# Optimization experiments

Measured on AMD Instinct MI355X. Metric: run time of the kernel, lower is better.

Reference implementation:

```python
import jax, jax.numpy as jnp
import numpy as np

L, B, E, H = 512, 32, 1024, 16
NEG = -1e9  # finite stand-in for masked_fill(-inf); avoids NaNs if a row were fully masked


def setup_inputs() -> dict:
    key = jax.random.key(0)
    ks = jax.random.split(key, 6)
    s_in = (2.0 / (3 * E + E)) ** 0.5   # xavier-ish scale for in_proj
    s_out = (2.0 / (E + E)) ** 0.5
    return {
        "query": jax.random.normal(ks[0], (L, B, E), jnp.float32),
        "key": jax.random.normal(ks[1], (L, B, E), jnp.float32),
        "value": jax.random.normal(ks[2], (L, B, E), jnp.float32),
        "attn_mask": jax.random.randint(ks[3], (B, L, L), 0, 2).astype(jnp.bool_),
        "in_proj_weight": jax.random.normal(ks[4], (3 * E, E), jnp.float32) * s_in,
        "in_proj_bias": jnp.zeros((3 * E,), jnp.float32),
        "out_proj_weight": jax.random.normal(ks[5], (E, E), jnp.float32) * s_out,
        "out_proj_bias": jnp.zeros((E,), jnp.float32),
        "num_heads": H,
    }


def reference(query, key, value, attn_mask, in_proj_weight, in_proj_bias,
              out_proj_weight, out_proj_bias, num_heads):
    Lq, Bz, Em = query.shape
    hd = Em // num_heads
    Wq, Wk, Wv = jnp.split(in_proj_weight, 3, axis=0)
    bq, bk, bv = jnp.split(in_proj_bias, 3, axis=0)
    # in-projection: x @ W^T + b  (torch F.linear convention)
    q = query @ Wq.T + bq
    k = key @ Wk.T + bk
    v = value @ Wv.T + bv
    # [L, B, E] -> [B*H, L, hd], batch-major (b*H + h) per torch view semantics
    def split_heads(x):
        return x.reshape(x.shape[0], Bz * num_heads, hd).transpose(1, 0, 2)
    q, k, v = split_heads(q), split_heads(k), split_heads(v)
    q = q / jnp.sqrt(jnp.asarray(hd, q.dtype))
    # scores: [B*H, Lq, Lk]
    attn = jnp.einsum('bqd,bkd->bqk', q, k)
    # mask broadcast to heads: [B, L, L] -> [B*H, L, L] with index b*H + h
    mask_mh = jnp.repeat(attn_mask, num_heads, axis=0)
    # original: scatter zeros where masked, then masked_fill(-inf) inside
    # multi_head_positional_attention; net effect = mask -> -inf before softmax
    attn = jnp.where(mask_mh, NEG, attn)
    p = jax.nn.softmax(attn, axis=-1)
    out = jnp.einsum('bqk,bkd->bqd', p, v)        # [B*H, Lq, hd]
    out = out.transpose(1, 0, 2).reshape(Lq, Bz, Em)
    out = out @ out_proj_weight.T + out_proj_bias  # [L, B, E]
    return out
```

## Files before the change

kernel.cpp:

```cpp
#include <hip/hip_runtime.h>
#include <hip/hip_bf16.h>
#include <stdint.h>

#define LSEQ 512
#define BATCH 32
#define EMB 1024
#define NHEAD 16
#define HDIM 64
#define TOK (LSEQ*BATCH)
#define BHTOT (BATCH*NHEAD)

typedef __attribute__((ext_vector_type(8))) short short8;
typedef __attribute__((ext_vector_type(4))) short short4v;
typedef __attribute__((ext_vector_type(4))) float f32x4;

__device__ __forceinline__ short f2bf(float f) {
  __hip_bfloat16 h = __float2bfloat16(f);
  union { __hip_bfloat16 h; short s; } u; u.h = h;
  return u.s;
}

#if defined(__has_builtin)
#if __has_builtin(__builtin_amdgcn_global_load_lds)
#define HAVE_GLL 1
#endif
#endif

__device__ __forceinline__ void gload_lds16(const void* g, void* l) {
#ifdef HAVE_GLL
  __builtin_amdgcn_global_load_lds((const __attribute__((address_space(1))) void*)g,
                                   (__attribute__((address_space(3))) void*)l, 16, 0, 0);
#else
  *(short8*)l = *(const short8*)g;
#endif
}

__global__ void cast_weights(const float* __restrict__ W, const float* __restrict__ Wo,
                             const float* __restrict__ bias,
                             short* __restrict__ Wb, short* __restrict__ Wob,
                             float* __restrict__ biasp)
{
  int i = blockIdx.x * 256 + threadIdx.x;
  if (i < 786432) {
    f32x4 v = ((const f32x4*)W)[i];
    int row = i >> 8;
    float s = (row < 1024) ? 0.125f : 1.0f;
    short4v o;
    o[0] = f2bf(v[0]*s); o[1] = f2bf(v[1]*s); o[2] = f2bf(v[2]*s); o[3] = f2bf(v[3]*s);
    ((short4v*)Wb)[i] = o;
  } else {
    int j = i - 786432;
    f32x4 v = ((const f32x4*)Wo)[j];
    short4v o;
    o[0] = f2bf(v[0]); o[1] = f2bf(v[1]); o[2] = f2bf(v[2]); o[3] = f2bf(v[3]);
    ((short4v*)Wob)[j] = o;
  }
  if (i < 768) {
    f32x4 v = ((const f32x4*)bias)[i];
    float s = (i < 256) ? 0.125f : 1.0f;
    f32x4 o = {v[0]*s, v[1]*s, v[2]*s, v[3]*s};
    ((f32x4*)biasp)[i] = o;
  }
}

__global__ void maskbits_kernel(const int* __restrict__ mask, uint32_t* __restrict__ mb)
{
  int w = (blockIdx.x * 256 + threadIdx.x) >> 6;
  int lane = threadIdx.x & 63;
  const int* src = mask + ((size_t)w << 9);
  uint32_t* dst = mb + w * 16;
  #pragma unroll
  for (int c = 0; c < 8; ++c) {
    int v = src[c * 64 + lane];
    unsigned long long m = __ballot(v != 0);
    if (lane == 0) dst[c*2]     = (uint32_t)m;
    if (lane == 1) dst[c*2 + 1] = (uint32_t)(m >> 32);
  }
}

__launch_bounds__(256, 4)
__global__ void proj_gemm(const float* __restrict__ Aq, const float* __restrict__ Ak,
                          const float* __restrict__ Av, const short* __restrict__ W,
                          const float* __restrict__ biasp,
                          short* __restrict__ qh, short* __restrict__ kh,
                          short* __restrict__ vh)
{
  int z = blockIdx.z;
  const float* A = (z == 0) ? Aq : (z == 1) ? Ak : Av;
  short* C       = (z == 0) ? qh : (z == 1) ? kh : vh;
  const short* B = W + (size_t)z * 1024 * 1024;
  const float* bp = biasp + z * 1024;

  int flat = blockIdx.y * 8 + blockIdx.x;
  int X = flat & 7, s = flat >> 3;
  int m0 = (X * 16 + (s >> 3)) * 128;
  int n0 = (s & 7) * 128;

  __shared__ alignas(16) short As[128 * 32];
  __shared__ alignas(16) short Bs[128 * 32];

  const int tid = threadIdx.x, lane = tid & 63;
  const int w = tid >> 6;
  const int wm = (w >> 1) * 64, wn = (w & 1) * 64;
  const int l15 = lane & 15, l4 = lane >> 4;

  f32x4 acc[4][4];
  #pragma unroll
  for (int mi = 0; mi < 4; ++mi)
    #pragma unroll
    for (int ni = 0; ni < 4; ++ni) acc[mi][ni] = f32x4{0.f, 0.f, 0.f, 0.f};

  for (int k0 = 0; k0 < 1024; k0 += 32) {
    __syncthreads();
    #pragma unroll
    for (int jj = 0; jj < 2; ++jj) {
      int ch = tid + jj * 256;
      int row = ch >> 2, cl = ch & 3;
      int sw = (row >> 1) & 3;
      int cs = cl ^ sw;
      const float* ga = A + (size_t)(m0 + row) * 1024 + k0 + cl * 8;
      f32x4 x0 = *(const f32x4*)ga;
      f32x4 x1 = *(const f32x4*)(ga + 4);
      short8 o;
      o[0] = f2bf(x0[0]); o[1] = f2bf(x0[1]); o[2] = f2bf(x0[2]); o[3] = f2bf(x0[3]);
      o[4] = f2bf(x1[0]); o[5] = f2bf(x1[1]); o[6] = f2bf(x1[2]); o[7] = f2bf(x1[3]);
      *(short8*)&As[row * 32 + cs * 8] = o;
      const short* gb = B + (size_t)(n0 + row) * 1024 + k0 + cs * 8;
      gload_lds16(gb, &Bs[ch * 8]);
    }
    __syncthreads();

    short8 af[4], bfr[4];
    #pragma unroll
    for (int mi = 0; mi < 4; ++mi) {
      int row = wm + mi * 16 + l15;
      int cs = l4 ^ ((row >> 1) & 3);
      af[mi] = *(const short8*)&As[row * 32 + cs * 8];
    }
    #pragma unroll
    for (int ni = 0; ni < 4; ++ni) {
      int row = wn + ni * 16 + l15;
      int cs = l4 ^ ((row >> 1) & 3);
      bfr[ni] = *(const short8*)&Bs[row * 32 + cs * 8];
    }
    #pragma unroll
    for (int mi = 0; mi < 4; ++mi)
      #pragma unroll
      for (int ni = 0; ni < 4; ++ni)
        acc[mi][ni] = __builtin_amdgcn_mfma_f32_16x16x32_bf16(af[mi], bfr[ni], acc[mi][ni], 0, 0, 0);
  }

  #pragma unroll
  for (int ni = 0; ni < 4; ++ni) {
    int gcol = n0 + wn + ni * 16 + l15;
    float bv = bp[gcol];
    int h = gcol >> 6, d = gcol & 63;
    #pragma unroll
    for (int mi = 0; mi < 4; ++mi) {
      int growb = m0 + wm + mi * 16 + l4 * 4;
      #pragma unroll
      for (int r = 0; r < 4; ++r) {
        int grow = growb + r;
        int lsq = grow >> 5, bb = grow & 31;
        C[((size_t)((bb * NHEAD + h) * LSEQ + lsq)) * HDIM + d] = f2bf(acc[mi][ni][r] + bv);
      }
    }
  }
}

__launch_bounds__(256, 2)
__global__ void attn_kernel(const short* __restrict__ qh, const short* __restrict__ kh,
                            const short* __restrict__ vh, const uint32_t* __restrict__ mb,
                            short* __restrict__ ao)
{
  int flat = blockIdx.y * 8 + blockIdx.x;
  int X = flat & 7, s = flat >> 3;
  int bh = X * 64 + (s >> 3);
  int qblk = s & 7;
  int b = bh >> 4, h = bh & 15;
  int q0 = qblk * 64;

  const int tid = threadIdx.x, lane = tid & 63, w = tid >> 6;
  const int l15 = lane & 15, l4 = lane >> 4;

  __shared__ alignas(16) short Ks[64 * 64];
  __shared__ alignas(16) short Vt[64 * 72];
  __shared__ alignas(16) short Ps[4 * 16 * 72];
  __shared__ uint32_t Mw[64 * 2];

  const size_t bhoff = (size_t)bh * (LSEQ * HDIM);

  short8 aq[2];
  {
    int qrow = q0 + w * 16 + l15;
    const short* qp = qh + bhoff + (size_t)qrow * HDIM + l4 * 8;
    aq[0] = *(const short8*)qp;
    aq[1] = *(const short8*)(qp + 32);
  }

  f32x4 oacc[4];
  #pragma unroll
  for (int n = 0; n < 4; ++n) oacc[n] = f32x4{0.f, 0.f, 0.f, 0.f};
  float m_i[4], l_i[4];
  #pragma unroll
  for (int r = 0; r < 4; ++r) { m_i[r] = -1e30f; l_i[r] = 0.f; }

  for (int kt = 0; kt < 8; ++kt) {
    __syncthreads();
    #pragma unroll
    for (int jj = 0; jj < 2; ++jj) {
      int ch = tid + jj * 256;
      int row = ch >> 3, cl = ch & 7;
      int cg = cl ^ (row & 7);
      const short* g = kh + bhoff + (size_t)(kt * 64 + row) * HDIM + cg * 8;
      gload_lds16(g, &Ks[ch * 8]);
    }
    #pragma unroll
    for (int jj = 0; jj < 2; ++jj) {
      int c = tid + jj * 256;
      int kv = c & 63, d0 = (c >> 6) * 8;
      const short* g = vh + bhoff + (size_t)(kt * 64 + kv) * HDIM + d0;
      short8 vv = *(const short8*)g;
      #pragma unroll
      for (int j = 0; j < 8; ++j) Vt[(d0 + j) * 72 + kv] = vv[j];
    }
    if (tid < 128) {
      int qr = tid >> 1, wd = tid & 1;
      Mw[qr * 2 + wd] = mb[((size_t)b * LSEQ + q0 + qr) * 16 + kt * 2 + wd];
    }
    __syncthreads();

    f32x4 sa[4];
    #pragma unroll
    for (int n = 0; n < 4; ++n) sa[n] = f32x4{0.f, 0.f, 0.f, 0.f};
    #pragma unroll
    for (int ss = 0; ss < 2; ++ss) {
      #pragma unroll
      for (int n = 0; n < 4; ++n) {
        int row = n * 16 + l15;
        int cs = (ss * 4 + l4) ^ (row & 7);
        short8 bk = *(const short8*)&Ks[row * 64 + cs * 8];
        sa[n] = __builtin_amdgcn_mfma_f32_16x16x32_bf16(aq[ss], bk, sa[n], 0, 0, 0);
      }
    }

    #pragma unroll
    for (int r = 0; r < 4; ++r) {
      int qr = w * 16 + l4 * 4 + r;
      uint32_t mlo = Mw[qr * 2], mhi = Mw[qr * 2 + 1];
      float sv[4];
      #pragma unroll
      for (int n = 0; n < 4; ++n) {
        int cc = n * 16 + l15;
        uint32_t bit = ((cc < 32 ? (mlo >> cc) : (mhi >> (cc - 32))) & 1u);
        sv[n] = bit ? -1e9f : sa[n][r];
      }
      float rmax = fmaxf(fmaxf(sv[0], sv[1]), fmaxf(sv[2], sv[3]));
      #pragma unroll
      for (int off = 1; off < 16; off <<= 1) rmax = fmaxf(rmax, __shfl_xor(rmax, off, 64));
      float mn = fmaxf(m_i[r], rmax);
      float sc = __expf(m_i[r] - mn);
      float p0 = __expf(sv[0] - mn), p1 = __expf(sv[1] - mn);
      float p2 = __expf(sv[2] - mn), p3 = __expf(sv[3] - mn);
      float rs = p0 + p1 + p2 + p3;
      #pragma unroll
      for (int off = 1; off < 16; off <<= 1) rs += __shfl_xor(rs, off, 64);
      l_i[r] = l_i[r] * sc + rs;
      m_i[r] = mn;
      #pragma unroll
      for (int n = 0; n < 4; ++n) oacc[n][r] *= sc;
      short* pp = &Ps[w * 1152 + (l4 * 4 + r) * 72];
      pp[0 * 16 + l15] = f2bf(p0);
      pp[1 * 16 + l15] = f2bf(p1);
      pp[2 * 16 + l15] = f2bf(p2);
      pp[3 * 16 + l15] = f2bf(p3);
    }

    #pragma unroll
    for (int ss = 0; ss < 2; ++ss) {
      short8 pa = *(const short8*)&Ps[w * 1152 + l15 * 72 + ss * 32 + l4 * 8];
      #pragma unroll
      for (int n = 0; n < 4; ++n) {
        short8 bv = *(const short8*)&Vt[(n * 16 + l15) * 72 + ss * 32 + l4 * 8];
        oacc[n] = __builtin_amdgcn_mfma_f32_16x16x32_bf16(pa, bv, oacc[n], 0, 0, 0);
      }
    }
  }

  #pragma unroll
  for (int r = 0; r < 4; ++r) {
    float inv = 1.0f / l_i[r];
    int qrow = q0 + w * 16 + l4 * 4 + r;
    size_t tbase = ((size_t)qrow * BATCH + b) * EMB + h * HDIM;
    #pragma unroll
    for (int n = 0; n < 4; ++n)
      ao[tbase + n * 16 + l15] = f2bf(oacc[n][r] * inv);
  }
}

__launch_bounds__(256, 4)
__global__ void out_gemm(const short* __restrict__ Ab, const short* __restrict__ W,
                         const float* __restrict__ bo, float* __restrict__ out)
{
  int flat = blockIdx.y * 8 + blockIdx.x;
  int X = flat & 7, s = flat >> 3;
  int m0 = (X * 16 + (s >> 3)) * 128;
  int n0 = (s & 7) * 128;

  __shared__ alignas(16) short As[128 * 32];
  __shared__ alignas(16) short Bs[128 * 32];

  const int tid = threadIdx.x, lane = tid & 63;
  const int w = tid >> 6;
  const int wm = (w >> 1) * 64, wn = (w & 1) * 64;
  const int l15 = lane & 15, l4 = lane >> 4;

  f32x4 acc[4][4];
  #pragma unroll
  for (int mi = 0; mi < 4; ++mi)
    #pragma unroll
    for (int ni = 0; ni < 4; ++ni) acc[mi][ni] = f32x4{0.f, 0.f, 0.f, 0.f};

  for (int k0 = 0; k0 < 1024; k0 += 32) {
    __syncthreads();
    #pragma unroll
    for (int jj = 0; jj < 2; ++jj) {
      int ch = tid + jj * 256;
      int row = ch >> 2, cl = ch & 3;
      int cs = cl ^ ((row >> 1) & 3);
      const short* ga = Ab + (size_t)(m0 + row) * 1024 + k0 + cs * 8;
      gload_lds16(ga, &As[ch * 8]);
      const short* gb = W + (size_t)(n0 + row) * 1024 + k0 + cs * 8;
      gload_lds16(gb, &Bs[ch * 8]);
    }
    __syncthreads();

    short8 af[4], bfr[4];
    #pragma unroll
    for (int mi = 0; mi < 4; ++mi) {
      int row = wm + mi * 16 + l15;
      int cs = l4 ^ ((row >> 1) & 3);
      af[mi] = *(const short8*)&As[row * 32 + cs * 8];
    }
    #pragma unroll
    for (int ni = 0; ni < 4; ++ni) {
      int row = wn + ni * 16 + l15;
      int cs = l4 ^ ((row >> 1) & 3);
      bfr[ni] = *(const short8*)&Bs[row * 32 + cs * 8];
    }
    #pragma unroll
    for (int mi = 0; mi < 4; ++mi)
      #pragma unroll
      for (int ni = 0; ni < 4; ++ni)
        acc[mi][ni] = __builtin_amdgcn_mfma_f32_16x16x32_bf16(af[mi], bfr[ni], acc[mi][ni], 0, 0, 0);
  }

  #pragma unroll
  for (int ni = 0; ni < 4; ++ni) {
    int gcol = n0 + wn + ni * 16 + l15;
    float bv = bo[gcol];
    #pragma unroll
    for (int mi = 0; mi < 4; ++mi) {
      int growb = m0 + wm + mi * 16 + l4 * 4;
      #pragma unroll
      for (int r = 0; r < 4; ++r)
        out[(size_t)(growb + r) * 1024 + gcol] = acc[mi][ni][r] + bv;
    }
  }
}

extern "C" void kernel_launch(void* const* d_in, const int* in_sizes, int n_in,
                              void* d_out, int out_size, void* d_ws, size_t ws_size,
                              hipStream_t stream) {
  const float* q_in = (const float*)d_in[0];
  const float* k_in = (const float*)d_in[1];
  const float* v_in = (const float*)d_in[2];
  const int*   mask = (const int*)d_in[3];
  const float* Wp   = (const float*)d_in[4];
  const float* bp   = (const float*)d_in[5];
  const float* Wo   = (const float*)d_in[6];
  const float* bo   = (const float*)d_in[7];

  char* ws = (char*)d_ws;
  short* Wb    = (short*)ws;    ws += (size_t)3072 * 1024 * 2;
  short* Wob   = (short*)ws;    ws += (size_t)1024 * 1024 * 2;
  float* biasp = (float*)ws;    ws += (size_t)3072 * 4;
  short* qh    = (short*)ws;    ws += (size_t)TOK * EMB * 2;
  short* kh    = (short*)ws;    ws += (size_t)TOK * EMB * 2;
  short* vh    = (short*)ws;    ws += (size_t)TOK * EMB * 2;
  short* ao    = (short*)ws;    ws += (size_t)TOK * EMB * 2;
  uint32_t* mb = (uint32_t*)ws; ws += (size_t)BATCH * LSEQ * 16 * 4;

  cast_weights<<<4096, 256, 0, stream>>>(Wp, Wo, bp, Wb, Wob, biasp);
  maskbits_kernel<<<4096, 256, 0, stream>>>(mask, mb);
  proj_gemm<<<dim3(8, 128, 3), 256, 0, stream>>>(q_in, k_in, v_in, Wb, biasp, qh, kh, vh);
  attn_kernel<<<dim3(8, 512), 256, 0, stream>>>(qh, kh, vh, mb, ao);
  out_gemm<<<dim3(8, 128), 256, 0, stream>>>(ao, Wob, bo, (float*)d_out);
}
```

Baseline: 357.7 us.

## Double-buffer LDS tiles in projection and output GEMMs to overlap loads with MFMA

Both projection and output GEMMs now use two LDS buffers per operand. The next K-slice is prefetched (global_load_lds for bf16 operands, register loads plus a deferred bf16 conversion for fp32 activations) while MFMAs run on the current buffer. This cuts one barrier per iteration and hides global memory latency. It doubles LDS use per block (32 KB), which may reduce occupancy under the 4-blocks-per-CU launch bound, and it holds more registers for the prefetched fp32 data.

```diff
diff --git a/kernel.cpp b/kernel.cpp
--- a/kernel.cpp
+++ b/kernel.cpp
@@ -18,6 +18,13 @@
   __hip_bfloat16 h = __float2bfloat16(f);
   union { __hip_bfloat16 h; short s; } u; u.h = h;
   return u.s;
+}
+
+__device__ __forceinline__ short8 cvt8(f32x4 x0, f32x4 x1) {
+  short8 o;
+  o[0] = f2bf(x0[0]); o[1] = f2bf(x0[1]); o[2] = f2bf(x0[2]); o[3] = f2bf(x0[3]);
+  o[4] = f2bf(x1[0]); o[5] = f2bf(x1[1]); o[6] = f2bf(x1[2]); o[7] = f2bf(x1[3]);
+  return o;
 }
 
 #if defined(__has_builtin)
@@ -96,58 +103,86 @@
   int m0 = (X * 16 + (s >> 3)) * 128;
   int n0 = (s & 7) * 128;
 
-  __shared__ alignas(16) short As[128 * 32];
-  __shared__ alignas(16) short Bs[128 * 32];
+  __shared__ alignas(16) short As[2][128 * 32];
+  __shared__ alignas(16) short Bs[2][128 * 32];
 
   const int tid = threadIdx.x, lane = tid & 63;
   const int w = tid >> 6;
   const int wm = (w >> 1) * 64, wn = (w & 1) * 64;
   const int l15 = lane & 15, l4 = lane >> 4;
 
+  const float* aSrc[2];
+  const short* bSrc[2];
+  int aDst[2], bDst[2];
+  #pragma unroll
+  for (int jj = 0; jj < 2; ++jj) {
+    int ch = tid + jj * 256;
+    int row = ch >> 2, cl = ch & 3;
+    int cs = cl ^ ((row >> 1) & 3);
+    aSrc[jj] = A + (size_t)(m0 + row) * 1024 + cl * 8;
+    bSrc[jj] = B + (size_t)(n0 + row) * 1024 + cs * 8;
+    aDst[jj] = row * 32 + cs * 8;
+    bDst[jj] = ch * 8;
+  }
+
   f32x4 acc[4][4];
   #pragma unroll
   for (int mi = 0; mi < 4; ++mi)
     #pragma unroll
     for (int ni = 0; ni < 4; ++ni) acc[mi][ni] = f32x4{0.f, 0.f, 0.f, 0.f};
 
+  #pragma unroll
+  for (int jj = 0; jj < 2; ++jj) {
+    f32x4 x0 = *(const f32x4*)(aSrc[jj]);
+    f32x4 x1 = *(const f32x4*)(aSrc[jj] + 4);
+    *(short8*)&As[0][aDst[jj]] = cvt8(x0, x1);
+    gload_lds16(bSrc[jj], &Bs[0][bDst[jj]]);
+  }
+  __syncthreads();
+
+  int cur = 0;
   for (int k0 = 0; k0 < 1024; k0 += 32) {
-    __syncthreads();
-    #pragma unroll
-    for (int jj = 0; jj < 2; ++jj) {
-      int ch = tid + jj * 256;
-      int row = ch >> 2, cl = ch & 3;
-      int sw = (row >> 1) & 3;
-      int cs = cl ^ sw;
-      const float* ga = A + (size_t)(m0 + row) * 1024 + k0 + cl * 8;
-      f32x4 x0 = *(const f32x4*)ga;
-      f32x4 x1 = *(const f32x4*)(ga + 4);
-      short8 o;
-      o[0] = f2bf(x0[0]); o[1] = f2bf(x0[1]); o[2] = f2bf(x0[2]); o[3] = f2bf(x0[3]);
-      o[4] = f2bf(x1[0]); o[5] = f2bf(x1[1]); o[6] = f2bf(x1[2]); o[7] = f2bf(x1[3]);
-      *(short8*)&As[row * 32 + cs * 8] = o;
-      const short* gb = B + (size_t)(n0 + row) * 1024 + k0 + cs * 8;
-      gload_lds16(gb, &Bs[ch * 8]);
-    }
-    __syncthreads();
+    const int nxt = cur ^ 1;
+    const bool has_next = (k0 + 32) < 1024;
+
+    f32x4 xa0[2], xa1[2];
+    if (has_next) {
+      #pragma unroll
+      for (int jj = 0; jj < 2; ++jj) {
+        xa0[jj] = *(const f32x4*)(aSrc[jj] + k0 + 32);
+        xa1[jj] = *(const f32x4*)(aSrc[jj] + k0 + 36);
+        gload_lds16(bSrc[jj] + k0 + 32, &Bs[nxt][bDst[jj]]);
+      }
+    }
 
     short8 af[4], bfr[4];
     #pragma unroll
     for (int mi = 0; mi < 4; ++mi) {
       int row = wm + mi * 16 + l15;
       int cs = l4 ^ ((row >> 1) & 3);
-      af[mi] = *(const short8*)&As[row * 32 + cs * 8];
+      af[mi] = *(const short8*)&As[cur][row * 32 + cs * 8];
     }
     #pragma unroll
     for (int ni = 0; ni < 4; ++ni) {
       int row = wn + ni * 16 + l15;
       int cs = l4 ^ ((row >> 1) & 3);
-      bfr[ni] = *(const short8*)&Bs[row * 32 + cs * 8];
-    }
+      bfr[ni] = *(const short8*)&Bs[cur][row * 32 + cs * 8];
+    }
+
     #pragma unroll
     for (int mi = 0; mi < 4; ++mi)
       #pragma unroll
       for (int ni = 0; ni < 4; ++ni)
         acc[mi][ni] = __builtin_amdgcn_mfma_f32_16x16x32_bf16(af[mi], bfr[ni], acc[mi][ni], 0, 0, 0);
+
+    if (has_next) {
+      #pragma unroll
+      for (int jj = 0; jj < 2; ++jj)
+        *(short8*)&As[nxt][aDst[jj]] = cvt8(xa0[jj], xa1[jj]);
+    }
+
+    __syncthreads();
+    cur = nxt;
   }
 
   #pragma unroll
@@ -307,52 +342,74 @@
   int m0 = (X * 16 + (s >> 3)) * 128;
   int n0 = (s & 7) * 128;
 
-  __shared__ alignas(16) short As[128 * 32];
-  __shared__ alignas(16) short Bs[128 * 32];
+  __shared__ alignas(16) short As[2][128 * 32];
+  __shared__ alignas(16) short Bs[2][128 * 32];
 
   const int tid = threadIdx.x, lane = tid & 63;
   const int w = tid >> 6;
   const int wm = (w >> 1) * 64, wn = (w & 1) * 64;
   const int l15 = lane & 15, l4 = lane >> 4;
 
+  const short* aSrc[2];
+  const short* bSrc[2];
+  int sDst[2];
+  #pragma unroll
+  for (int jj = 0; jj < 2; ++jj) {
+    int ch = tid + jj * 256;
+    int row = ch >> 2, cl = ch & 3;
+    int cs = cl ^ ((row >> 1) & 3);
+    aSrc[jj] = Ab + (size_t)(m0 + row) * 1024 + cs * 8;
+    bSrc[jj] = W + (size_t)(n0 + row) * 1024 + cs * 8;
+    sDst[jj] = ch * 8;
+  }
+
   f32x4 acc[4][4];
   #pragma unroll
   for (int mi = 0; mi < 4; ++mi)
     #pragma unroll
     for (int ni = 0; ni < 4; ++ni) acc[mi][ni] = f32x4{0.f, 0.f, 0.f, 0.f};
 
+  #pragma unroll
+  for (int jj = 0; jj < 2; ++jj) {
+    gload_lds16(aSrc[jj], &As[0][sDst[jj]]);
+    gload_lds16(bSrc[jj], &Bs[0][sDst[jj]]);
+  }
+  __syncthreads();
+
+  int cur = 0;
   for (int k0 = 0; k0 < 1024; k0 += 32) {
-    __syncthreads();
-    #pragma unroll
-    for (int jj = 0; jj < 2; ++jj) {
-      int ch = tid + jj * 256;
-      int row = ch >> 2, cl = ch & 3;
-      int cs = cl ^ ((row >> 1) & 3);
-      const short* ga = Ab + (size_t)(m0 + row) * 1024 + k0 + cs * 8;
-      gload_lds16(ga, &As[ch * 8]);
-      const short* gb = W + (size_t)(n0 + row) * 1024 + k0 + cs * 8;
-      gload_lds16(gb, &Bs[ch * 8]);
-    }
-    __syncthreads();
+    const int nxt = cur ^ 1;
+    const bool has_next = (k0 + 32) < 1024;
+
+    if (has_next) {
+      #pragma unroll
+      for (int jj = 0; jj < 2; ++jj) {
+        gload_lds16(aSrc[jj] + k0 + 32, &As[nxt][sDst[jj]]);
+        gload_lds16(bSrc[jj] + k0 + 32, &Bs[nxt][sDst[jj]]);
+      }
+    }
 
     short8 af[4], bfr[4];
     #pragma unroll
     for (int mi = 0; mi < 4; ++mi) {
       int row = wm + mi * 16 + l15;
       int cs = l4 ^ ((row >> 1) & 3);
-      af[mi] = *(const short8*)&As[row * 32 + cs * 8];
+      af[mi] = *(const short8*)&As[cur][row * 32 + cs * 8];
     }
     #pragma unroll
     for (int ni = 0; ni < 4; ++ni) {
       int row = wn + ni * 16 + l15;
       int cs = l4 ^ ((row >> 1) & 3);
-      bfr[ni] = *(const short8*)&Bs[row * 32 + cs * 8];
+      bfr[ni] = *(const short8*)&Bs[cur][row * 32 + cs * 8];
     }
     #pragma unroll
     for (int mi = 0; mi < 4; ++mi)
       #pragma unroll
       for (int ni = 0; ni < 4; ++ni)
         acc[mi][ni] = __builtin_amdgcn_mfma_f32_16x16x32_bf16(af[mi], bfr[ni], acc[mi][ni], 0, 0, 0);
+
+    __syncthreads();
+    cur = nxt;
   }
 
   #pragma unroll
```

Result: slower. 365.7 us (+2.2%).

## Pre-cast activations to bf16 and triple-buffer GEMM loads via direct-to-LDS

Applied to the files above, without the earlier changes.

A new pass casts query, key and value to bf16 up front, so the projection GEMM can load both operands with global_load_lds instead of converting fp32 in the main loop. Both GEMMs now use a three-stage LDS ring driven by explicit vmcnt waits, keeping loads for upcoming k-slices in flight while MFMAs run. The cost is an extra full read and write of the activations, three times the LDS per block, and occupancy lowered from 4 to 3 blocks. The ao buffer reuses the xb region, which is safe because the projection has finished before attention writes it.

```diff
diff --git a/kernel.cpp b/kernel.cpp
--- a/kernel.cpp
+++ b/kernel.cpp
@@ -33,6 +33,29 @@
 #else
   *(short8*)l = *(const short8*)g;
 #endif
+}
+
+#define WAIT_VM8  do { asm volatile("s_waitcnt vmcnt(8)" ::: "memory"); __builtin_amdgcn_sched_barrier(0); } while (0)
+#define WAIT_VM4  do { asm volatile("s_waitcnt vmcnt(4)" ::: "memory"); __builtin_amdgcn_sched_barrier(0); } while (0)
+#define WAIT_VM0  do { asm volatile("s_waitcnt vmcnt(0)" ::: "memory"); __builtin_amdgcn_sched_barrier(0); } while (0)
+#define WAIT_LGKM0 do { asm volatile("s_waitcnt lgkmcnt(0)" ::: "memory"); __builtin_amdgcn_sched_barrier(0); } while (0)
+#define BAR() __builtin_amdgcn_s_barrier()
+
+__global__ void castx_kernel(const float* __restrict__ xq, const float* __restrict__ xk,
+                             const float* __restrict__ xv, short* __restrict__ xb)
+{
+  const int stride = 4096 * 256;
+  int base = blockIdx.x * 256 + threadIdx.x;
+  #pragma unroll
+  for (int it = 0; it < 12; ++it) {
+    int i = base + it * stride;
+    const float* src = (i < 4194304) ? xq : (i < 8388608) ? xk : xv;
+    int j = i & 4194303;
+    f32x4 v = ((const f32x4*)src)[j];
+    short4v o;
+    o[0] = f2bf(v[0]); o[1] = f2bf(v[1]); o[2] = f2bf(v[2]); o[3] = f2bf(v[3]);
+    ((short4v*)xb)[i] = o;
+  }
 }
 
 __global__ void cast_weights(const float* __restrict__ W, const float* __restrict__ Wo,
@@ -78,77 +101,116 @@
   }
 }
 
-__launch_bounds__(256, 4)
-__global__ void proj_gemm(const float* __restrict__ Aq, const float* __restrict__ Ak,
-                          const float* __restrict__ Av, const short* __restrict__ W,
+
+#define FRAG_READ(AsX, BsX)                                           \
+    short8 af[4], bfr[4];                                             \
+    _Pragma("unroll")                                                 \
+    for (int mi = 0; mi < 4; ++mi) {                                  \
+      int row = wm + mi * 16 + l15;                                   \
+      int cs = l4 ^ ((row >> 1) & 3);                                 \
+      af[mi] = *(const short8*)&AsX[row * 32 + cs * 8];               \
+    }                                                                 \
+    _Pragma("unroll")                                                 \
+    for (int ni = 0; ni < 4; ++ni) {                                  \
+      int row = wn + ni * 16 + l15;                                   \
+      int cs = l4 ^ ((row >> 1) & 3);                                 \
+      bfr[ni] = *(const short8*)&BsX[row * 32 + cs * 8];              \
+    }
+
+#define DO_MFMA()                                                     \
+    _Pragma("unroll")                                                 \
+    for (int mi = 0; mi < 4; ++mi)                                    \
+      _Pragma("unroll")                                               \
+      for (int ni = 0; ni < 4; ++ni)                                  \
+        acc[mi][ni] = __builtin_amdgcn_mfma_f32_16x16x32_bf16(af[mi], bfr[ni], acc[mi][ni], 0, 0, 0)
+
+#define ISSUE(AsX, BsX, koff)                                         \
+    _Pragma("unroll")                                                 \
+    for (int jj = 0; jj < 2; ++jj) {                                  \
+      gload_lds16(aSrc[jj] + (koff), &AsX[sDst[jj]]);                 \
+      gload_lds16(bSrc[jj] + (koff), &BsX[sDst[jj]]);                 \
+    }
+
+#define GSTEP_I(AsX, BsX, WAITM, koff)                                \
+  { WAITM; BAR();                                                     \
+    FRAG_READ(AsX, BsX);                                              \
+    WAIT_LGKM0; BAR();                                                \
+    ISSUE(AsX, BsX, koff);                                            \
+    DO_MFMA(); }
+
+#define GSTEP_N(AsX, BsX, WAITM)                                      \
+  { WAITM; BAR();                                                     \
+    FRAG_READ(AsX, BsX);                                              \
+    WAIT_LGKM0; BAR();                                                \
+    DO_MFMA(); }
+
+#define STAGE_COORDS(Abase, Bbase)                                    \
+  const short* aSrc[2]; const short* bSrc[2]; int sDst[2];            \
+  _Pragma("unroll")                                                   \
+  for (int jj = 0; jj < 2; ++jj) {                                    \
+    int ch = tid + jj * 256;                                          \
+    int row = ch >> 2, cl = ch & 3;                                   \
+    int cs = cl ^ ((row >> 1) & 3);                                   \
+    aSrc[jj] = (Abase) + (size_t)(m0 + row) * 1024 + cs * 8;          \
+    bSrc[jj] = (Bbase) + (size_t)(n0 + row) * 1024 + cs * 8;          \
+    sDst[jj] = ch * 8;                                                \
+  }
+
+#define PIPE_BODY()                                                   \
+        \
+  ISSUE(As0, Bs0, 0); ISSUE(As1, Bs1, 32); ISSUE(As2, Bs2, 64);       \
+                \
+  for (int i = 0; i < 9; ++i) {                                       \
+    const int s = 3 * i;                                              \
+    GSTEP_I(As0, Bs0, WAIT_VM8, (s + 3) * 32);                        \
+    GSTEP_I(As1, Bs1, WAIT_VM8, (s + 4) * 32);                        \
+    GSTEP_I(As2, Bs2, WAIT_VM8, (s + 5) * 32);                        \
+  }                                                                   \
+           \
+  GSTEP_I(As0, Bs0, WAIT_VM8, 30 * 32);                               \
+  GSTEP_I(As1, Bs1, WAIT_VM8, 31 * 32);                               \
+  GSTEP_N(As2, Bs2, WAIT_VM8);                                        \
+  GSTEP_N(As0, Bs0, WAIT_VM4);                                        \
+  GSTEP_N(As1, Bs1, WAIT_VM0);
+
+__launch_bounds__(256, 3)
+__global__ void proj_gemm(const short* __restrict__ xb, const short* __restrict__ W,
                           const float* __restrict__ biasp,
                           short* __restrict__ qh, short* __restrict__ kh,
                           short* __restrict__ vh)
 {
   int z = blockIdx.z;
-  const float* A = (z == 0) ? Aq : (z == 1) ? Ak : Av;
+  const short* A = xb + (size_t)z * TOK * EMB;
   short* C       = (z == 0) ? qh : (z == 1) ? kh : vh;
   const short* B = W + (size_t)z * 1024 * 1024;
   const float* bp = biasp + z * 1024;
 
   int flat = blockIdx.y * 8 + blockIdx.x;
-  int X = flat & 7, s = flat >> 3;
-  int m0 = (X * 16 + (s >> 3)) * 128;
-  int n0 = (s & 7) * 128;
-
-  __shared__ alignas(16) short As[128 * 32];
-  __shared__ alignas(16) short Bs[128 * 32];
+  int X = flat & 7, s0 = flat >> 3;
+  int m0 = (X * 16 + (s0 >> 3)) * 128;
+  int n0 = (s0 & 7) * 128;
+
+  __shared__ alignas(16) short As0[128 * 32];
+  __shared__ alignas(16) short As1[128 * 32];
+  __shared__ alignas(16) short As2[128 * 32];
+  __shared__ alignas(16) short Bs0[128 * 32];
+  __shared__ alignas(16) short Bs1[128 * 32];
+  __shared__ alignas(16) short Bs2[128 * 32];
 
   const int tid = threadIdx.x, lane = tid & 63;
   const int w = tid >> 6;
   const int wm = (w >> 1) * 64, wn = (w & 1) * 64;
   const int l15 = lane & 15, l4 = lane >> 4;
 
+  STAGE_COORDS(A, B);
+
   f32x4 acc[4][4];
   #pragma unroll
   for (int mi = 0; mi < 4; ++mi)
     #pragma unroll
     for (int ni = 0; ni < 4; ++ni) acc[mi][ni] = f32x4{0.f, 0.f, 0.f, 0.f};
 
-  for (int k0 = 0; k0 < 1024; k0 += 32) {
-    __syncthreads();
-    #pragma unroll
-    for (int jj = 0; jj < 2; ++jj) {
-      int ch = tid + jj * 256;
-      int row = ch >> 2, cl = ch & 3;
-      int sw = (row >> 1) & 3;
-      int cs = cl ^ sw;
-      const float* ga = A + (size_t)(m0 + row) * 1024 + k0 + cl * 8;
-      f32x4 x0 = *(const f32x4*)ga;
-      f32x4 x1 = *(const f32x4*)(ga + 4);
-      short8 o;
-      o[0] = f2bf(x0[0]); o[1] = f2bf(x0[1]); o[2] = f2bf(x0[2]); o[3] = f2bf(x0[3]);
-      o[4] = f2bf(x1[0]); o[5] = f2bf(x1[1]); o[6] = f2bf(x1[2]); o[7] = f2bf(x1[3]);
-      *(short8*)&As[row * 32 + cs * 8] = o;
-      const short* gb = B + (size_t)(n0 + row) * 1024 + k0 + cs * 8;
-      gload_lds16(gb, &Bs[ch * 8]);
-    }
-    __syncthreads();
-
-    short8 af[4], bfr[4];
-    #pragma unroll
-    for (int mi = 0; mi < 4; ++mi) {
-      int row = wm + mi * 16 + l15;
-      int cs = l4 ^ ((row >> 1) & 3);
-      af[mi] = *(const short8*)&As[row * 32 + cs * 8];
-    }
-    #pragma unroll
-    for (int ni = 0; ni < 4; ++ni) {
-      int row = wn + ni * 16 + l15;
-      int cs = l4 ^ ((row >> 1) & 3);
-      bfr[ni] = *(const short8*)&Bs[row * 32 + cs * 8];
-    }
-    #pragma unroll
-    for (int mi = 0; mi < 4; ++mi)
-      #pragma unroll
-      for (int ni = 0; ni < 4; ++ni)
-        acc[mi][ni] = __builtin_amdgcn_mfma_f32_16x16x32_bf16(af[mi], bfr[ni], acc[mi][ni], 0, 0, 0);
-  }
+  PIPE_BODY();
 
   #pragma unroll
   for (int ni = 0; ni < 4; ++ni) {
@@ -164,6 +226,51 @@
         int lsq = grow >> 5, bb = grow & 31;
         C[((size_t)((bb * NHEAD + h) * LSEQ + lsq)) * HDIM + d] = f2bf(acc[mi][ni][r] + bv);
       }
+    }
+  }
+}
+
+__launch_bounds__(256, 3)
+__global__ void out_gemm(const short* __restrict__ Ab, const short* __restrict__ W,
+                         const float* __restrict__ bo, float* __restrict__ out)
+{
+  int flat = blockIdx.y * 8 + blockIdx.x;
+  int X = flat & 7, s0 = flat >> 3;
+  int m0 = (X * 16 + (s0 >> 3)) * 128;
+  int n0 = (s0 & 7) * 128;
+
+  __shared__ alignas(16) short As0[128 * 32];
+  __shared__ alignas(16) short As1[128 * 32];
+  __shared__ alignas(16) short As2[128 * 32];
+  __shared__ alignas(16) short Bs0[128 * 32];
+  __shared__ alignas(16) short Bs1[128 * 32];
+  __shared__ alignas(16) short Bs2[128 * 32];
+
+  const int tid = threadIdx.x, lane = tid & 63;
+  const int w = tid >> 6;
+  const int wm = (w >> 1) * 64, wn = (w & 1) * 64;
+  const int l15 = lane & 15, l4 = lane >> 4;
+
+  STAGE_COORDS(Ab, W);
+
+  f32x4 acc[4][4];
+  #pragma unroll
+  for (int mi = 0; mi < 4; ++mi)
+    #pragma unroll
+    for (int ni = 0; ni < 4; ++ni) acc[mi][ni] = f32x4{0.f, 0.f, 0.f, 0.f};
+
+  PIPE_BODY();
+
+  #pragma unroll
+  for (int ni = 0; ni < 4; ++ni) {
+    int gcol = n0 + wn + ni * 16 + l15;
+    float bv = bo[gcol];
+    #pragma unroll
+    for (int mi = 0; mi < 4; ++mi) {
+      int growb = m0 + wm + mi * 16 + l4 * 4;
+      #pragma unroll
+      for (int r = 0; r < 4; ++r)
+        out[(size_t)(growb + r) * 1024 + gcol] = acc[mi][ni][r] + bv;
     }
   }
 }
@@ -295,77 +402,6 @@
     #pragma unroll
     for (int n = 0; n < 4; ++n)
       ao[tbase + n * 16 + l15] = f2bf(oacc[n][r] * inv);
-  }
-}
-
-__launch_bounds__(256, 4)
-__global__ void out_gemm(const short* __restrict__ Ab, const short* __restrict__ W,
-                         const float* __restrict__ bo, float* __restrict__ out)
-{
-  int flat = blockIdx.y * 8 + blockIdx.x;
-  int X = flat & 7, s = flat >> 3;
-  int m0 = (X * 16 + (s >> 3)) * 128;
-  int n0 = (s & 7) * 128;
-
-  __shared__ alignas(16) short As[128 * 32];
-  __shared__ alignas(16) short Bs[128 * 32];
-
-  const int tid = threadIdx.x, lane = tid & 63;
-  const int w = tid >> 6;
-  const int wm = (w >> 1) * 64, wn = (w & 1) * 64;
-  const int l15 = lane & 15, l4 = lane >> 4;
-
-  f32x4 acc[4][4];
-  #pragma unroll
-  for (int mi = 0; mi < 4; ++mi)
-    #pragma unroll
-    for (int ni = 0; ni < 4; ++ni) acc[mi][ni] = f32x4{0.f, 0.f, 0.f, 0.f};
-
-  for (int k0 = 0; k0 < 1024; k0 += 32) {
-    __syncthreads();
-    #pragma unroll
-    for (int jj = 0; jj < 2; ++jj) {
-      int ch = tid + jj * 256;
-      int row = ch >> 2, cl = ch & 3;
-      int cs = cl ^ ((row >> 1) & 3);
-      const short* ga = Ab + (size_t)(m0 + row) * 1024 + k0 + cs * 8;
-      gload_lds16(ga, &As[ch * 8]);
-      const short* gb = W + (size_t)(n0 + row) * 1024 + k0 + cs * 8;
-      gload_lds16(gb, &Bs[ch * 8]);
-    }
-    __syncthreads();
-
-    short8 af[4], bfr[4];
-    #pragma unroll
-    for (int mi = 0; mi < 4; ++mi) {
-      int row = wm + mi * 16 + l15;
-      int cs = l4 ^ ((row >> 1) & 3);
-      af[mi] = *(const short8*)&As[row * 32 + cs * 8];
-    }
-    #pragma unroll
-    for (int ni = 0; ni < 4; ++ni) {
-      int row = wn + ni * 16 + l15;
-      int cs = l4 ^ ((row >> 1) & 3);
-      bfr[ni] = *(const short8*)&Bs[row * 32 + cs * 8];
-    }
-    #pragma unroll
-    for (int mi = 0; mi < 4; ++mi)
-      #pragma unroll
-      for (int ni = 0; ni < 4; ++ni)
-        acc[mi][ni] = __builtin_amdgcn_mfma_f32_16x16x32_bf16(af[mi], bfr[ni], acc[mi][ni], 0, 0, 0);
-  }
-
-  #pragma unroll
-  for (int ni = 0; ni < 4; ++ni) {
-    int gcol = n0 + wn + ni * 16 + l15;
-    float bv = bo[gcol];
-    #pragma unroll
-    for (int mi = 0; mi < 4; ++mi) {
-      int growb = m0 + wm + mi * 16 + l4 * 4;
-      #pragma unroll
-      for (int r = 0; r < 4; ++r)
-        out[(size_t)(growb + r) * 1024 + gcol] = acc[mi][ni][r] + bv;
-    }
   }
 }
 
@@ -385,15 +421,17 @@
   short* Wb    = (short*)ws;    ws += (size_t)3072 * 1024 * 2;
   short* Wob   = (short*)ws;    ws += (size_t)1024 * 1024 * 2;
   float* biasp = (float*)ws;    ws += (size_t)3072 * 4;
+  uint32_t* mb = (uint32_t*)ws; ws += (size_t)BATCH * LSEQ * 16 * 4;
   short* qh    = (short*)ws;    ws += (size_t)TOK * EMB * 2;
   short* kh    = (short*)ws;    ws += (size_t)TOK * EMB * 2;
   short* vh    = (short*)ws;    ws += (size_t)TOK * EMB * 2;
-  short* ao    = (short*)ws;    ws += (size_t)TOK * EMB * 2;
-  uint32_t* mb = (uint32_t*)ws; ws += (size_t)BATCH * LSEQ * 16 * 4;
-
+  short* xb    = (short*)ws;    ws += (size_t)3 * TOK * EMB * 2;
+  short* ao    = xb;
+
+  castx_kernel<<<4096, 256, 0, stream>>>(q_in, k_in, v_in, xb);
   cast_weights<<<4096, 256, 0, stream>>>(Wp, Wo, bp, Wb, Wob, biasp);
   maskbits_kernel<<<4096, 256, 0, stream>>>(mask, mb);
-  proj_gemm<<<dim3(8, 128, 3), 256, 0, stream>>>(q_in, k_in, v_in, Wb, biasp, qh, kh, vh);
+  proj_gemm<<<dim3(8, 128, 3), 256, 0, stream>>>(xb, Wb, biasp, qh, kh, vh);
   attn_kernel<<<dim3(8, 512), 256, 0, stream>>>(qh, kh, vh, mb, ao);
   out_gemm<<<dim3(8, 128), 256, 0, stream>>>(ao, Wob, bo, (float*)d_out);
 }
```

Measured after the change: 372.5 us. 1.04x slower.
